# Performance work log

Measured on AMD Instinct MI355X. Metric: run time of the kernel, lower is better.

Reference implementation:

```python
import jax, jax.numpy as jnp
import numpy as np

H = 1024

def setup_inputs() -> dict:
    key = jax.random.key(0)
    ks = jax.random.split(key, 10)
    B, T = 64, 256
    s = 1.0 / np.sqrt(H)  # torch LSTM init scale (uniform(-1/sqrt(H), 1/sqrt(H)))
    return {
        "x": jax.random.normal(ks[0], (B, T, H), jnp.float32),
        "h0": jax.random.normal(ks[1], (1, B, H), jnp.float32),
        "c0": jax.random.normal(ks[2], (1, B, H), jnp.float32),
        "dones": jax.random.randint(ks[3], (B, T), 0, 2).astype(bool),
        "W_ih": jax.random.uniform(ks[4], (4 * H, H), jnp.float32, -s, s),
        "W_hh": jax.random.uniform(ks[5], (4 * H, H), jnp.float32, -s, s),
        "b_ih": jax.random.uniform(ks[6], (4 * H,), jnp.float32, -s, s),
        "b_hh": jax.random.uniform(ks[7], (4 * H,), jnp.float32, -s, s),
    }


def reference(x, h0, c0, dones, W_ih, W_hh, b_ih, b_hh):
    # x: [B,T,H]; h0,c0: [1,B,H]; dones: [B,T] bool
    B, T, _ = x.shape
    xs = jnp.transpose(x, (1, 0, 2))          # [T,B,H]
    ds = jnp.transpose(dones, (1, 0))         # [T,B]
    # Precompute input projections for all steps in one big GEMM
    x_proj = jnp.einsum('tbh,gh->tbg', xs, W_ih) + b_ih + b_hh  # [T,B,4H]

    def step(carry, inp):
        h, c = carry                          # [B,H] each
        xp, done_t = inp                      # [B,4H], [B]
        gates = xp + h @ W_hh.T               # [B,4H]
        i, f, g, o = jnp.split(gates, 4, axis=-1)
        i = jax.nn.sigmoid(i)
        f = jax.nn.sigmoid(f)
        g = jnp.tanh(g)
        o = jax.nn.sigmoid(o)
        c_new = f * c + i * g
        h_new = o * jnp.tanh(c_new)
        # done-based reset applies AFTER emitting the step output
        mask = (~done_t)[:, None].astype(h_new.dtype)
        return (h_new * mask, c_new * mask), h_new

    (h_f, c_f), ys = jax.lax.scan(step, (h0[0], c0[0]), (x_proj, ds))
    out = jnp.tanh(jnp.transpose(ys, (1, 0, 2)))  # activation, [B,T,H]
    return out, h_f[None], c_f[None]
```

## Files before the change

kernel.cpp:

```cpp
#include <hip/hip_runtime.h>

typedef __attribute__((ext_vector_type(8))) short short8;
typedef __attribute__((ext_vector_type(4))) float f32x4;
typedef unsigned long long ull;

__device__ __forceinline__ unsigned short f2bf(float f){
  union { float f; unsigned u; } v; v.f = f;
  return (unsigned short)((v.u + 0x7FFFu + ((v.u >> 16) & 1u)) >> 16);
}
__device__ __forceinline__ float bf2f(unsigned short u){
  union { unsigned u; float f; } v; v.u = ((unsigned)u) << 16; return v.f;
}
__device__ __forceinline__ float fsig(float x){ return 1.f / (1.f + __expf(-x)); }
__device__ __forceinline__ float ftanh(float x){ return 1.f - 2.f / (__expf(2.f * x) + 1.f); }

__device__ __forceinline__ void gld16(const void* g, void* l){
  __builtin_amdgcn_global_load_lds((const __attribute__((address_space(1))) void*)g,
                                   (__attribute__((address_space(3))) void*)l, 16, 0, 0);
}

__global__ __launch_bounds__(256) void cast_x_kernel(const float* __restrict__ x,
                                                     unsigned short* __restrict__ xT){
  const int row = blockIdx.x;
  const int b = row >> 8, t = row & 255;
  float4 v = ((const float4*)(x + (size_t)row * 1024))[threadIdx.x];
  ushort4 o; o.x = f2bf(v.x); o.y = f2bf(v.y); o.z = f2bf(v.z); o.w = f2bf(v.w);
  ((ushort4*)(xT + (size_t)(t * 64 + b) * 1024))[threadIdx.x] = o;
}

__global__ __launch_bounds__(256) void cast_rows_kernel(const float* __restrict__ s,
                                                        unsigned short* __restrict__ d){
  const size_t i = (size_t)blockIdx.x * 256 + threadIdx.x;
  float4 v = ((const float4*)s)[i];
  ushort4 o; o.x = f2bf(v.x); o.y = f2bf(v.y); o.z = f2bf(v.z); o.w = f2bf(v.w);
  ((ushort4*)d)[i] = o;
}

__global__ __launch_bounds__(256) void gemm_xproj_kernel(
    const unsigned short* __restrict__ A,
    const unsigned short* __restrict__ W,
    const float* __restrict__ bih,
    const float* __restrict__ bhh,
    unsigned short* __restrict__ C){
  __shared__ __align__(16) unsigned short As[2][4096];
  __shared__ __align__(16) unsigned short Bs[2][4096];
  const int tid  = threadIdx.x;
  const int lane = tid & 63;
  const int wv   = tid >> 6;
  const int wr   = wv >> 1, wc = wv & 1;
  const int mBase = blockIdx.y << 7;
  const int nBase = blockIdx.x << 7;
  const int lg4 = lane >> 4, lg15 = lane & 15;

  f32x4 acc[4][4] = {};

  auto stage = [&](int buf, int kk){
    #pragma unroll
    for (int rnd = 0; rnd < 2; ++rnd){
      const int s    = tid + (rnd << 8);
      const int row  = s >> 2;
      const int q    = s & 3;
      const int slog = q ^ (row & 3);
      const size_t col = (size_t)(kk << 5) + (slog << 3);
      unsigned short* dA = &As[buf][(size_t)((wv << 6) + (rnd << 8)) << 3];
      unsigned short* dB = &Bs[buf][(size_t)((wv << 6) + (rnd << 8)) << 3];
      gld16(A + (size_t)(mBase + row) * 1024 + col, dA);
      gld16(W + (size_t)(nBase + row) * 1024 + col, dB);
    }
  };

  stage(0, 0);
  __syncthreads();

  for (int kk = 0; kk < 32; ++kk){
    const int buf = kk & 1;
    if (kk != 31) stage(buf ^ 1, kk + 1);
    short8 af[4], bfr[4];
    #pragma unroll
    for (int mi = 0; mi < 4; ++mi){
      const int row = (wr << 6) + (mi << 4) + lg15;
      const int q   = lg4 ^ (row & 3);
      af[mi] = *(const short8*)&As[buf][(row << 5) + (q << 3)];
    }
    #pragma unroll
    for (int ni = 0; ni < 4; ++ni){
      const int row = (wc << 6) + (ni << 4) + lg15;
      const int q   = lg4 ^ (row & 3);
      bfr[ni] = *(const short8*)&Bs[buf][(row << 5) + (q << 3)];
    }
    #pragma unroll
    for (int mi = 0; mi < 4; ++mi)
      #pragma unroll
      for (int ni = 0; ni < 4; ++ni)
        acc[mi][ni] = __builtin_amdgcn_mfma_f32_16x16x32_bf16(af[mi], bfr[ni], acc[mi][ni], 0, 0, 0);
    __syncthreads();
  }

  #pragma unroll
  for (int ni = 0; ni < 4; ++ni){
    const int gcol = nBase + (wc << 6) + (ni << 4) + lg15;
    const float bsum = bih[gcol] + bhh[gcol];
    const int g = gcol >> 10, kk = gcol & 1023;
    const int ktt = kk >> 4, kc = kk & 15;
    #pragma unroll
    for (int mi = 0; mi < 4; ++mi){
      const int grow0 = mBase + (wr << 6) + (mi << 4) + (lg4 << 2);
      const int t = grow0 >> 6, b = grow0 & 63;
      const int btt = b >> 4, rb0 = b & 15;
      const size_t base = ((size_t)((t * 4 + btt) * 64 + ktt) << 10)
                          + (g << 8) + (rb0 << 4) + kc;
      #pragma unroll
      for (int r = 0; r < 4; ++r)
        C[base + (r << 4)] = f2bf(acc[mi][ni][r] + bsum);
    }
  }
}

__global__ __launch_bounds__(64) void lstm_steps_kernel(
    const float* __restrict__ Whh,
    const unsigned short* __restrict__ xproj,
    const float* __restrict__ h0,
    const float* __restrict__ c0,
    const int* __restrict__ dones,
    unsigned short* __restrict__ hbuf,
    float* __restrict__ out,
    unsigned* __restrict__ bar){
  __shared__ __align__(16) unsigned short Ws[64 * 1024];
  const int lane = threadIdx.x;
  const int bt = blockIdx.x >> 6;
  const int kt = blockIdx.x & 63;
  const int b0 = bt << 4, k0 = kt << 4;
  const int l15 = lane & 15;
  const int l4  = lane >> 4;
  unsigned* cnt = bar + (bt << 6);

  {
    const int i = (kt << 6) + lane;
    const int row = i >> 8;
    const int c4 = (i & 255) << 2;
    float4 v = *(const float4*)(h0 + (size_t)(b0 + row) * 1024 + c4);
    union { ull q; unsigned short s[4]; } p;
    p.s[0] = f2bf(v.x); p.s[1] = f2bf(v.y); p.s[2] = f2bf(v.z); p.s[3] = f2bf(v.w);
    __hip_atomic_store((ull*)hbuf + (size_t)(b0 + row) * 256 + (c4 >> 2), p.q,
                       __ATOMIC_RELAXED, __HIP_MEMORY_SCOPE_AGENT);
  }
  asm volatile("s_waitcnt vmcnt(0)" ::: "memory");
  if (lane == 0)
    __hip_atomic_fetch_add(cnt, 1u, __ATOMIC_RELAXED, __HIP_MEMORY_SCOPE_AGENT);

  {
    const int wrow = lane;
    const int g = lane >> 4, j = lane & 15;
    const float* src = Whh + ((size_t)(g << 10) + k0 + j) * 1024;
    for (int c = 0; c < 1024; c += 8){
      float4 v0 = *(const float4*)(src + c);
      float4 v1 = *(const float4*)(src + c + 4);
      short8 pk;
      pk[0] = (short)f2bf(v0.x); pk[1] = (short)f2bf(v0.y);
      pk[2] = (short)f2bf(v0.z); pk[3] = (short)f2bf(v0.w);
      pk[4] = (short)f2bf(v1.x); pk[5] = (short)f2bf(v1.y);
      pk[6] = (short)f2bf(v1.z); pk[7] = (short)f2bf(v1.w);
      const int q = (c >> 3) ^ (wrow & 7);
      *(short8*)&Ws[(wrow << 10) + (q << 3)] = pk;
    }
  }

  ull pk0, pk1, pk2, pk3;
  {
    const int* dp = dones + (size_t)(b0 + l15) * 256 + (l4 << 6);
    ull w = 0;
    for (int j = 0; j < 64; ++j) w |= ((ull)(dp[j] != 0)) << j;
    pk0 = __shfl(w, l15);
    pk1 = __shfl(w, 16 + l15);
    pk2 = __shfl(w, 32 + l15);
    pk3 = __shfl(w, 48 + l15);
  }

  float creg[4];
  {
    float4 cv = *(const float4*)(c0 + (size_t)(b0 + l15) * 1024 + k0 + (l4 << 2));
    creg[0] = cv.x; creg[1] = cv.y; creg[2] = cv.z; creg[3] = cv.w;
  }

  const ull* xpb = (const ull*)xproj;
  ull xpc[4];
  {
    const size_t ch0 = ((size_t)(bt * 64 + kt)) << 8;
    #pragma unroll
    for (int g = 0; g < 4; ++g) xpc[g] = xpb[ch0 + (g << 6) + (l15 << 2) + l4];
  }

  union AV { ull q[2]; short8 v; };

  #pragma unroll
  for (int qq = 0; qq < 4; ++qq){
    const ull pkq = (qq == 0) ? pk0 : (qq == 1) ? pk1 : (qq == 2) ? pk2 : pk3;
    for (int t2 = 0; t2 < 64; ++t2){
      const int t = (qq << 6) + t2;
      const ull* hc = (const ull*)hbuf + ((size_t)(t & 1) << 14);
      ull* hn = (ull*)hbuf + ((size_t)((t + 1) & 1) << 14);

      if (lane == 0){
        const unsigned tgt = ((unsigned)t + 1u) << 6;
        while (__hip_atomic_load(cnt, __ATOMIC_RELAXED, __HIP_MEMORY_SCOPE_AGENT) < tgt)
          __builtin_amdgcn_s_sleep(1);
      }
      asm volatile("" ::: "memory");

      const ull* hrow = hc + (size_t)(b0 + l15) * 256 + (l4 << 1);
      AV ha[8], hbv[8];
      auto load8 = [&](AV (&hv)[8], int kb){
        #pragma unroll
        for (int j = 0; j < 8; ++j){
          const int ks = (kb << 3) + j;
          hv[j].q[0] = __hip_atomic_load(hrow + (ks << 3),     __ATOMIC_RELAXED, __HIP_MEMORY_SCOPE_AGENT);
          hv[j].q[1] = __hip_atomic_load(hrow + (ks << 3) + 1, __ATOMIC_RELAXED, __HIP_MEMORY_SCOPE_AGENT);
        }
      };
      f32x4 acc[4];
      auto accinit = [&](){
        #pragma unroll
        for (int g = 0; g < 4; ++g){
          union { ull q; unsigned short s[4]; } u; u.q = xpc[g];
          #pragma unroll
          for (int r = 0; r < 4; ++r) acc[g][r] = bf2f(u.s[r]);
        }
      };
      auto consume = [&](AV (&hv)[8], int kb){
        #pragma unroll
        for (int j = 0; j < 8; ++j){
          const int ks = (kb << 3) + j;
          #pragma unroll
          for (int g = 0; g < 4; ++g){
            const int wrow = (g << 4) + l15;
            const int qs = ((ks << 2) + l4) ^ (wrow & 7);
            const short8 wf = *(const short8*)&Ws[(wrow << 10) + (qs << 3)];
            acc[g] = __builtin_amdgcn_mfma_f32_16x16x32_bf16(wf, hv[j].v, acc[g], 0, 0, 0);
          }
        }
      };
      load8(ha, 0); load8(hbv, 1);
      accinit();
      consume(ha, 0); load8(ha, 2);
      consume(hbv, 1); load8(hbv, 3);
      consume(ha, 2); consume(hbv, 3);

      const float m = ((pkq >> t2) & 1ull) ? 0.f : 1.f;
      float ot4[4], hm4[4];
      unsigned short hb16[4];
      #pragma unroll
      for (int r = 0; r < 4; ++r){
        const float ig = fsig(acc[0][r]);
        const float fg = fsig(acc[1][r]);
        const float gg = ftanh(acc[2][r]);
        const float og = fsig(acc[3][r]);
        const float cn = fg * creg[r] + ig * gg;
        const float hv = og * ftanh(cn);
        ot4[r] = ftanh(hv);
        creg[r] = cn * m;
        const float hm = hv * m;
        hm4[r] = hm;
        hb16[r] = f2bf(hm);
      }

      {
        union { ull q; unsigned short s[4]; } p;
        p.s[0] = hb16[0]; p.s[1] = hb16[1]; p.s[2] = hb16[2]; p.s[3] = hb16[3];
        __hip_atomic_store(hn + (size_t)(b0 + l15) * 256 + (k0 >> 2) + l4, p.q,
                           __ATOMIC_RELAXED, __HIP_MEMORY_SCOPE_AGENT);
      }
      asm volatile("s_waitcnt vmcnt(0)" ::: "memory");
      if (lane == 0)
        __hip_atomic_fetch_add(cnt, 1u, __ATOMIC_RELAXED, __HIP_MEMORY_SCOPE_AGENT);

      *(float4*)(out + (size_t)(b0 + l15) * 262144 + ((size_t)t << 10) + k0 + (l4 << 2))
          = make_float4(ot4[0], ot4[1], ot4[2], ot4[3]);
      if (t == 255){
        float* hf = out + 16777216 + (size_t)(b0 + l15) * 1024 + k0 + (l4 << 2);
        float* cf = out + 16842752 + (size_t)(b0 + l15) * 1024 + k0 + (l4 << 2);
        *(float4*)hf = make_float4(hm4[0], hm4[1], hm4[2], hm4[3]);
        *(float4*)cf = make_float4(creg[0], creg[1], creg[2], creg[3]);
      }
      {
        const int tn = (t < 255) ? t + 1 : 255;
        const size_t chn = ((size_t)((tn * 4 + bt) * 64 + kt)) << 8;
        #pragma unroll
        for (int g = 0; g < 4; ++g) xpc[g] = xpb[chn + (g << 6) + (l15 << 2) + l4];
      }
    }
  }
}

extern "C" void kernel_launch(void* const* d_in, const int* in_sizes, int n_in,
                              void* d_out, int out_size, void* d_ws, size_t ws_size,
                              hipStream_t stream){
  const float* x    = (const float*)d_in[0];
  const float* h0   = (const float*)d_in[1];
  const float* c0   = (const float*)d_in[2];
  const int*   dn   = (const int*)d_in[3];
  const float* Wih  = (const float*)d_in[4];
  const float* Whh  = (const float*)d_in[5];
  const float* bih  = (const float*)d_in[6];
  const float* bhh  = (const float*)d_in[7];
  float* out = (float*)d_out;
  char* ws = (char*)d_ws;

  unsigned short* xT    = (unsigned short*)(ws);
  unsigned short* Wib   = (unsigned short*)(ws + 33554432);
  unsigned short* xproj = (unsigned short*)(ws + 41943040);
  unsigned short* hbuf  = (unsigned short*)(ws + 176160768);
  unsigned*       bar   = (unsigned*)(ws + 176422912);

  cast_x_kernel<<<16384, 256, 0, stream>>>(x, xT);
  cast_rows_kernel<<<4096, 256, 0, stream>>>(Wih, Wib);
  gemm_xproj_kernel<<<dim3(32, 128), 256, 0, stream>>>(xT, Wib, bih, bhh, xproj);
  hipMemsetAsync(bar, 0, 1024, stream);

  const float* Whh_ = Whh; const unsigned short* xp_ = xproj;
  const float* h0_ = h0; const float* c0_ = c0; const int* dn_ = dn;
  unsigned short* hb_ = hbuf; float* out_ = out; unsigned* bar_ = bar;
  void* args[] = {&Whh_, &xp_, &h0_, &c0_, &dn_, &hb_, &out_, &bar_};
  hipError_t ce = hipLaunchCooperativeKernel((void*)lstm_steps_kernel, dim3(256), dim3(64),
                                             args, 0, stream);
  if (ce != hipSuccess){
    lstm_steps_kernel<<<256, 64, 0, stream>>>(Whh_, xp_, h0_, c0_, dn_, hb_, out_, bar_);
  }
}
```

Measured before the change: 1.399 ms.

## Split per-batch step barrier into eight sub-counters and poll halves separately

The single per-batch-tile arrival counter is replaced by eight counters, each padded to its own 256-byte slot and shared by a group of eight k-tiles. Each block now waits in two stages: it polls the four counters covering the first half of the hidden dimension and starts its MFMAs on that half, then polls the second half. The products for the two halves go into separate accumulators that are summed before the activations. This is meant to reduce atomic contention on one address and let compute on early-arriving h chunks overlap with waiting for the rest, at the cost of more polling traffic and a few extra registers.

```diff
diff --git a/kernel.cpp b/kernel.cpp
--- a/kernel.cpp
+++ b/kernel.cpp
@@ -132,7 +132,8 @@
   const int b0 = bt << 4, k0 = kt << 4;
   const int l15 = lane & 15;
   const int l4  = lane >> 4;
-  unsigned* cnt = bar + (bt << 6);
+  unsigned* cnt = bar + (bt << 9);
+  unsigned* mycnt = cnt + ((kt >> 3) << 6);
 
   {
     const int i = (kt << 6) + lane;
@@ -146,7 +147,7 @@
   }
   asm volatile("s_waitcnt vmcnt(0)" ::: "memory");
   if (lane == 0)
-    __hip_atomic_fetch_add(cnt, 1u, __ATOMIC_RELAXED, __HIP_MEMORY_SCOPE_AGENT);
+    __hip_atomic_fetch_add(mycnt, 1u, __ATOMIC_RELAXED, __HIP_MEMORY_SCOPE_AGENT);
 
   {
     const int wrow = lane;
@@ -191,6 +192,15 @@
   }
 
   union AV { ull q[2]; short8 v; };
+  auto pollHalf = [&](int half, unsigned tgt){
+    const unsigned* cp = cnt + (((half << 2) + (lane & 3)) << 6);
+    unsigned v = __hip_atomic_load(cp, __ATOMIC_RELAXED, __HIP_MEMORY_SCOPE_AGENT);
+    while (!__all((int)(v >= tgt))){
+      __builtin_amdgcn_s_sleep(1);
+      v = __hip_atomic_load(cp, __ATOMIC_RELAXED, __HIP_MEMORY_SCOPE_AGENT);
+    }
+    asm volatile("" ::: "memory");
+  };
 
   #pragma unroll
   for (int qq = 0; qq < 4; ++qq){
@@ -199,16 +209,10 @@
       const int t = (qq << 6) + t2;
       const ull* hc = (const ull*)hbuf + ((size_t)(t & 1) << 14);
       ull* hn = (ull*)hbuf + ((size_t)((t + 1) & 1) << 14);
-
-      if (lane == 0){
-        const unsigned tgt = ((unsigned)t + 1u) << 6;
-        while (__hip_atomic_load(cnt, __ATOMIC_RELAXED, __HIP_MEMORY_SCOPE_AGENT) < tgt)
-          __builtin_amdgcn_s_sleep(1);
-      }
-      asm volatile("" ::: "memory");
+      const unsigned tgt = ((unsigned)t + 1u) << 3;
 
       const ull* hrow = hc + (size_t)(b0 + l15) * 256 + (l4 << 1);
-      AV ha[8], hbv[8];
+      AV h0v[8], h1v[8], h2v[8], h3v[8];
       auto load8 = [&](AV (&hv)[8], int kb){
         #pragma unroll
         for (int j = 0; j < 8; ++j){
@@ -217,16 +221,8 @@
           hv[j].q[1] = __hip_atomic_load(hrow + (ks << 3) + 1, __ATOMIC_RELAXED, __HIP_MEMORY_SCOPE_AGENT);
         }
       };
-      f32x4 acc[4];
-      auto accinit = [&](){
-        #pragma unroll
-        for (int g = 0; g < 4; ++g){
-          union { ull q; unsigned short s[4]; } u; u.q = xpc[g];
-          #pragma unroll
-          for (int r = 0; r < 4; ++r) acc[g][r] = bf2f(u.s[r]);
-        }
-      };
-      auto consume = [&](AV (&hv)[8], int kb){
+      f32x4 accP[4], accQ[4];
+      auto consume = [&](AV (&hv)[8], int kb, f32x4 (&acc)[4]){
         #pragma unroll
         for (int j = 0; j < 8; ++j){
           const int ks = (kb << 3) + j;
@@ -239,21 +235,33 @@
           }
         }
       };
-      load8(ha, 0); load8(hbv, 1);
-      accinit();
-      consume(ha, 0); load8(ha, 2);
-      consume(hbv, 1); load8(hbv, 3);
-      consume(ha, 2); consume(hbv, 3);
+
+      pollHalf(0, tgt);
+      load8(h0v, 0); load8(h1v, 1);
+      #pragma unroll
+      for (int g = 0; g < 4; ++g){
+        union { ull q; unsigned short s[4]; } u; u.q = xpc[g];
+        #pragma unroll
+        for (int r = 0; r < 4; ++r) accP[g][r] = bf2f(u.s[r]);
+        accQ[g][0] = 0.f; accQ[g][1] = 0.f; accQ[g][2] = 0.f; accQ[g][3] = 0.f;
+      }
+      consume(h0v, 0, accP);
+
+      pollHalf(1, tgt);
+      load8(h2v, 2); load8(h3v, 3);
+      consume(h1v, 1, accP);
+      consume(h2v, 2, accQ);
+      consume(h3v, 3, accQ);
 
       const float m = ((pkq >> t2) & 1ull) ? 0.f : 1.f;
       float ot4[4], hm4[4];
       unsigned short hb16[4];
       #pragma unroll
       for (int r = 0; r < 4; ++r){
-        const float ig = fsig(acc[0][r]);
-        const float fg = fsig(acc[1][r]);
-        const float gg = ftanh(acc[2][r]);
-        const float og = fsig(acc[3][r]);
+        const float ig = fsig(accP[0][r] + accQ[0][r]);
+        const float fg = fsig(accP[1][r] + accQ[1][r]);
+        const float gg = ftanh(accP[2][r] + accQ[2][r]);
+        const float og = fsig(accP[3][r] + accQ[3][r]);
         const float cn = fg * creg[r] + ig * gg;
         const float hv = og * ftanh(cn);
         ot4[r] = ftanh(hv);
@@ -271,7 +279,7 @@
       }
       asm volatile("s_waitcnt vmcnt(0)" ::: "memory");
       if (lane == 0)
-        __hip_atomic_fetch_add(cnt, 1u, __ATOMIC_RELAXED, __HIP_MEMORY_SCOPE_AGENT);
+        __hip_atomic_fetch_add(mycnt, 1u, __ATOMIC_RELAXED, __HIP_MEMORY_SCOPE_AGENT);
 
       *(float4*)(out + (size_t)(b0 + l15) * 262144 + ((size_t)t << 10) + k0 + (l4 << 2))
           = make_float4(ot4[0], ot4[1], ot4[2], ot4[3]);
@@ -314,7 +322,7 @@
   cast_x_kernel<<<16384, 256, 0, stream>>>(x, xT);
   cast_rows_kernel<<<4096, 256, 0, stream>>>(Wih, Wib);
   gemm_xproj_kernel<<<dim3(32, 128), 256, 0, stream>>>(xT, Wib, bih, bhh, xproj);
-  hipMemsetAsync(bar, 0, 1024, stream);
+  hipMemsetAsync(bar, 0, 8192, stream);
 
   const float* Whh_ = Whh; const unsigned short* xp_ = xproj;
   const float* h0_ = h0; const float* c0_ = c0; const int* dn_ = dn;
```

New measurement: 1.916 ms. 36.9% more time.
